# Kernel optimization log

Hardware: AMD Instinct MI355X
Metric: run time of the kernel (lower is better)

The kernel has to match this reference:

```python
import jax, jax.numpy as jnp
import numpy as np
from math import sqrt

B, IN_F, OUT_F = 32, 1024, 4096
DROPOUT_RATE = 0.1


def setup_inputs() -> dict:
    key = jax.random.key(0)
    kx, kw, kb, kmw, kmb = jax.random.split(key, 5)
    k = sqrt(1.0 / IN_F)  # He-style init std from source
    x = jax.random.normal(kx, (B, IN_F), dtype=jnp.float32)
    weight = k * jax.random.normal(kw, (IN_F, OUT_F), dtype=jnp.float32)
    bias = k * jax.random.normal(kb, (OUT_F,), dtype=jnp.float32)
    # per-sample Bernoulli keep masks: rand > dropout_rate (no 1/(1-p) rescale in source)
    w_mask = jax.random.uniform(kmw, (B, IN_F, OUT_F)) > DROPOUT_RATE
    b_mask = jax.random.uniform(kmb, (B, OUT_F)) > DROPOUT_RATE
    return {"x": x, "weight": weight, "bias": bias, "w_mask": w_mask, "b_mask": b_mask}


def reference(x, weight, bias, w_mask, b_mask):
    # 'w' dropout mode: per-sample masked weight matmul, vectorized over batch
    # (replaces the original Python loop of B GEMVs with one batched contraction).
    mw = w_mask.astype(x.dtype)
    y = jnp.einsum("bi,io,bio->bo", x, weight, mw)  # [B, OUT_F]
    return y + bias[None, :] * b_mask.astype(x.dtype)
```

## Files before the change

### kernel.cpp

```cpp
#include <hip/hip_runtime.h>
#include <hip/hip_bf16.h>


#define B_DIM 32
#define IN_F 1024
#define OUT_F 4096

__global__ __launch_bounds__(256) void dropout_linear_kernel(
    const float* __restrict__ x,
    const float* __restrict__ weight,
    const float* __restrict__ bias,
    const int* __restrict__ w_mask,
    const int* __restrict__ b_mask,
    float* __restrict__ out)
{
    const int tid = blockIdx.x * blockDim.x + threadIdx.x;
    const int o = tid & (OUT_F - 1);
    const int b = tid >> 12;

    __shared__ float xs[IN_F];
    const float* xrow = x + b * IN_F;
    for (int i = threadIdx.x; i < IN_F; i += 256) {
        xs[i] = xrow[i];
    }
    __syncthreads();

    const int* __restrict__ mcol =
        w_mask + (size_t)b * (size_t)IN_F * (size_t)OUT_F + o;
    const float* __restrict__ wcol = weight + o;

    float acc = 0.0f;
#pragma unroll 8
    for (int i = 0; i < IN_F; ++i) {
        const float xi = xs[i];
        const float wi = wcol[(size_t)i * OUT_F];
        const float mi = (float)mcol[(size_t)i * OUT_F];
        acc = fmaf(xi * mi, wi, acc);
    }

    const float bm = (float)b_mask[tid];
    out[tid] = fmaf(bias[o], bm, acc);
}

extern "C" void kernel_launch(void* const* d_in, const int* in_sizes, int n_in,
                              void* d_out, int out_size, void* d_ws, size_t ws_size,
                              hipStream_t stream) {
    const float* x      = (const float*)d_in[0];
    const float* weight = (const float*)d_in[1];
    const float* bias   = (const float*)d_in[2];
    const int*   w_mask = (const int*)d_in[3];
    const int*   b_mask = (const int*)d_in[4];
    float* out = (float*)d_out;

    const int total = B_DIM * OUT_F;
    dropout_linear_kernel<<<total / 256, 256, 0, stream>>>(
        x, weight, bias, w_mask, b_mask, out);
}
```

Before: 680.0 us.

## Split reduction dimension across blocks with vectorized loads and separate reduce kernel

Splits the IN_F reduction into 16 chunks so there are 2048 blocks instead of 512, each thread handling four outputs with int4/float4 loads. Per-chunk partial sums go to the workspace, and a second kernel sums them and adds the masked bias. The goal is more parallelism and wider memory transactions on the mask stream, which is about 512MB and bandwidth bound. The cost is an extra launch plus 8MB of partial-sum writes and reads.

```diff
diff --git a/kernel.cpp b/kernel.cpp
--- a/kernel.cpp
+++ b/kernel.cpp
@@ -1,45 +1,63 @@
 #include <hip/hip_runtime.h>
-#include <hip/hip_bf16.h>
 
 
 #define B_DIM 32
 #define IN_F 1024
 #define OUT_F 4096
+#define N_CHUNK 16
+#define I_CHUNK (IN_F / N_CHUNK)
+#define O_PER_BLK 1024
+#define BO (B_DIM * OUT_F)
 
-__global__ __launch_bounds__(256) void dropout_linear_kernel(
+__global__ __launch_bounds__(256, 4) void masked_gemv_partial(
     const float* __restrict__ x,
     const float* __restrict__ weight,
+    const int* __restrict__ w_mask,
+    float* __restrict__ partial)
+{
+    const int bid   = blockIdx.x;
+    const int b     = bid >> 6;
+    const int s     = bid & 63;
+    const int o_blk = s >> 4;
+    const int chunk = s & 15;
+    const int i0    = chunk * I_CHUNK;
+    const int o     = o_blk * O_PER_BLK + (threadIdx.x << 2);
+
+    __shared__ float xs[I_CHUNK];
+    if (threadIdx.x < I_CHUNK) xs[threadIdx.x] = x[b * IN_F + i0 + threadIdx.x];
+    __syncthreads();
+
+    const int*   mptr = w_mask + (size_t)b * IN_F * OUT_F + (size_t)i0 * OUT_F + o;
+    const float* wptr = weight + (size_t)i0 * OUT_F + o;
+
+    float4 acc = {0.f, 0.f, 0.f, 0.f};
+#pragma unroll 8
+    for (int i = 0; i < I_CHUNK; ++i) {
+        const float xi = xs[i];
+        const int4   m = *(const int4*)  (mptr + (size_t)i * OUT_F);
+        const float4 w = *(const float4*)(wptr + (size_t)i * OUT_F);
+        acc.x = fmaf(xi * (float)m.x, w.x, acc.x);
+        acc.y = fmaf(xi * (float)m.y, w.y, acc.y);
+        acc.z = fmaf(xi * (float)m.z, w.z, acc.z);
+        acc.w = fmaf(xi * (float)m.w, w.w, acc.w);
+    }
+
+    *(float4*)(partial + (size_t)chunk * BO + b * OUT_F + o) = acc;
+}
+
+__global__ __launch_bounds__(256) void reduce_bias_kernel(
+    const float* __restrict__ partial,
     const float* __restrict__ bias,
-    const int* __restrict__ w_mask,
     const int* __restrict__ b_mask,
     float* __restrict__ out)
 {
-    const int tid = blockIdx.x * blockDim.x + threadIdx.x;
+    const int tid = blockIdx.x * 256 + threadIdx.x;
+    float s = 0.f;
+#pragma unroll
+    for (int c = 0; c < N_CHUNK; ++c)
+        s += partial[(size_t)c * BO + tid];
     const int o = tid & (OUT_F - 1);
-    const int b = tid >> 12;
-
-    __shared__ float xs[IN_F];
-    const float* xrow = x + b * IN_F;
-    for (int i = threadIdx.x; i < IN_F; i += 256) {
-        xs[i] = xrow[i];
-    }
-    __syncthreads();
-
-    const int* __restrict__ mcol =
-        w_mask + (size_t)b * (size_t)IN_F * (size_t)OUT_F + o;
-    const float* __restrict__ wcol = weight + o;
-
-    float acc = 0.0f;
-#pragma unroll 8
-    for (int i = 0; i < IN_F; ++i) {
-        const float xi = xs[i];
-        const float wi = wcol[(size_t)i * OUT_F];
-        const float mi = (float)mcol[(size_t)i * OUT_F];
-        acc = fmaf(xi * mi, wi, acc);
-    }
-
-    const float bm = (float)b_mask[tid];
-    out[tid] = fmaf(bias[o], bm, acc);
+    out[tid] = fmaf(bias[o], (float)b_mask[tid], s);
 }
 
 extern "C" void kernel_launch(void* const* d_in, const int* in_sizes, int n_in,
@@ -50,9 +68,9 @@
     const float* bias   = (const float*)d_in[2];
     const int*   w_mask = (const int*)d_in[3];
     const int*   b_mask = (const int*)d_in[4];
-    float* out = (float*)d_out;
+    float* out     = (float*)d_out;
+    float* partial = (float*)d_ws;
 
-    const int total = B_DIM * OUT_F;
-    dropout_linear_kernel<<<total / 256, 256, 0, stream>>>(
-        x, weight, bias, w_mask, b_mask, out);
+    masked_gemv_partial<<<B_DIM * 64, 256, 0, stream>>>(x, weight, w_mask, partial);
+    reduce_bias_kernel<<<BO / 256, 256, 0, stream>>>(partial, bias, b_mask, out);
 }
```

New measurement: 702.8 us. 3.3% more time.
